# Kernel tuning notes

Hardware: AMD Instinct MI355X
Metric: run time of the kernel (lower is better)

Reference implementation:

```python
import jax, jax.numpy as jnp
import numpy as np

DIM = 1024
NUM_HEADS = 16
HEAD_DIM = DIM // NUM_HEADS


def setup_inputs() -> dict:
    key = jax.random.key(0)
    k1, k2, k3 = jax.random.split(key, 3)
    x = jax.random.normal(k1, (2, 2048, DIM), dtype=jnp.float32)
    # nn.Linear weights stored as [out, in]; apply as x @ W.T
    w_qkv = jax.random.normal(k2, (3 * DIM, DIM), dtype=jnp.float32) * (1.0 / np.sqrt(DIM))
    w_out = jax.random.normal(k3, (DIM, DIM), dtype=jnp.float32) * (1.0 / np.sqrt(DIM))
    return {"x": x, "w_qkv": w_qkv, "w_out": w_out}


def reference(x, w_qkv, w_out):
    b, t, _ = x.shape
    qkv = x @ w_qkv.T                                  # [b, t, 3*dim]
    qkv = qkv.reshape(b, t, 3, NUM_HEADS, HEAD_DIM)    # (three h d) split order
    q, k, v = jnp.moveaxis(qkv, 2, 0)                  # each [b, t, h, d]
    q = q.transpose(0, 2, 1, 3)                        # [b, h, t, d]
    k = k.transpose(0, 2, 1, 3)
    v = v.transpose(0, 2, 1, 3)
    attn = jnp.einsum('bhid,bhjd->bhij', q, k) / np.sqrt(HEAD_DIM)
    causal_mask = jnp.triu(jnp.ones((t, t), dtype=bool), k=1)
    attn = jnp.where(causal_mask, -jnp.inf, attn)
    attn = jax.nn.softmax(attn, axis=-1)
    out = jnp.einsum('bhij,bhjd->bhid', attn, v)
    out = out.transpose(0, 2, 1, 3).reshape(b, t, DIM)
    return out @ w_out.T
```

## Files before the change

### kernel.cpp

```cpp
#include <hip/hip_runtime.h>

#define DIM_ 1024
#define HEADS_ 16
#define HD_ 64
#define T_ 2048
#define BATCH_ 2
#define QKVN_ 3072

typedef unsigned short u16;
typedef unsigned int u32;
typedef float f32x4 __attribute__((ext_vector_type(4)));
typedef float f32x16 __attribute__((ext_vector_type(16)));
typedef short s16x8 __attribute__((ext_vector_type(8)));
typedef unsigned short u16x4 __attribute__((ext_vector_type(4)));

__device__ __forceinline__ u16 f2bf(float f) {
  unsigned u = __float_as_uint(f);
  u += 0x7fffu + ((u >> 16) & 1u);
  return (u16)(u >> 16);
}

__device__ __forceinline__ float fexp2(float x) {
  float r;
  asm("v_exp_f32 %0, %1" : "=v"(r) : "v"(x));
  return r;
}

__device__ __forceinline__ float fmax3(float a, float b, float c) {
  float r;
  asm("v_max3_f32 %0, %1, %2, %3" : "=v"(r) : "v"(a), "v"(b), "v"(c));
  return r;
}

__device__ __forceinline__ u32 cvtpk(float a, float b) {
  u32 r;
  asm("v_cvt_pk_bf16_f32 %0, %1, %2" : "=v"(r) : "v"(a), "v"(b));
  return r;
}

__global__ __launch_bounds__(256) void cvt_all(const float* __restrict__ x,
                                               const float* __restrict__ wqkv,
                                               const float* __restrict__ wout,
                                               u16* __restrict__ outbase) {
  int i = blockIdx.x * 256 + threadIdx.x;
  const float4* src;
  int off;
  if (i < 1048576) { src = (const float4*)x; off = i; }
  else if (i < 1835008) { src = (const float4*)wqkv; off = i - 1048576; }
  else { src = (const float4*)wout; off = i - 1835008; }
  float4 v = src[off];
  u16x4 o;
  o.x = f2bf(v.x); o.y = f2bf(v.y); o.z = f2bf(v.z); o.w = f2bf(v.w);
  reinterpret_cast<u16x4*>(outbase)[i] = o;
}

__device__ __forceinline__ void gld_lds16(const void* g, void* l) {
  auto gp = (__attribute__((address_space(1))) char*)(unsigned long long)g;
  auto lp = (__attribute__((address_space(3))) char*)(unsigned int)(unsigned long long)l;
  __builtin_amdgcn_global_load_lds(gp, lp, 16, 0, 0);
}

template <int MODE>
__global__ __launch_bounds__(256) void gemm1(const u16* __restrict__ A,
                                             const u16* __restrict__ B,
                                             void* __restrict__ Cv,
                                             u16* __restrict__ vto) {
  constexpr int K = 1024;
  constexpr int NN = (MODE == 1) ? 1024 : QKVN_;
  constexpr int NT = (MODE == 1) ? 8 : 24;
  constexpr int CPX = (MODE == 1) ? 32 : 96;
  __shared__ __align__(16) u16 smem[16384];
  u16* As = smem;
  u16* Bs = smem + 8192;
  const int bid = blockIdx.x;
  const int wk = (bid & 7) * CPX + (bid >> 3);
  const int mt = wk / NT, nt = wk % NT;
  const int tid = threadIdx.x;
  const int lane = tid & 63;
  const int w = tid >> 6;
  const int wr = w >> 1, wc = w & 1;
  const int lrow = lane & 15, kg = lane >> 4;
  const u16* Ag = A + (size_t)(mt * 128) * K;
  const u16* Bg = B + (size_t)(nt * 128) * K;

  f32x4 acc[4][4];
#pragma unroll
  for (int i = 0; i < 4; ++i)
#pragma unroll
    for (int j = 0; j < 4; ++j) {
      f32x4 z = {0.f, 0.f, 0.f, 0.f};
      acc[i][j] = z;
    }

  const int srow = tid >> 3;
  const int scol = 8 * ((tid & 7) ^ ((tid >> 3) & 7));
  const int ldsw = (tid & ~63) * 16;

  int aoff[4][2], boff[4][2];
#pragma unroll
  for (int mf = 0; mf < 4; ++mf)
#pragma unroll
    for (int ks = 0; ks < 2; ++ks) {
      aoff[mf][ks] = (wr * 64 + mf * 16 + lrow) * 128 + (((ks * 4 + kg) ^ (lrow & 7)) << 4);
      boff[mf][ks] = (wc * 64 + mf * 16 + lrow) * 128 + (((ks * 4 + kg) ^ (lrow & 7)) << 4);
    }

  for (int k0 = 0; k0 < K; k0 += 64) {
#pragma unroll
    for (int c = 0; c < 4; ++c) {
      gld_lds16(Ag + (size_t)(c * 32 + srow) * K + k0 + scol, (char*)As + c * 4096 + ldsw);
      gld_lds16(Bg + (size_t)(c * 32 + srow) * K + k0 + scol, (char*)Bs + c * 4096 + ldsw);
    }
    __syncthreads();
#pragma unroll
    for (int ks = 0; ks < 2; ++ks) {
      s16x8 a[4], b[4];
#pragma unroll
      for (int mf = 0; mf < 4; ++mf)
        a[mf] = *(const s16x8*)((const char*)As + aoff[mf][ks]);
#pragma unroll
      for (int nf = 0; nf < 4; ++nf)
        b[nf] = *(const s16x8*)((const char*)Bs + boff[nf][ks]);
#pragma unroll
      for (int mf = 0; mf < 4; ++mf)
#pragma unroll
        for (int nf = 0; nf < 4; ++nf)
          acc[mf][nf] = __builtin_amdgcn_mfma_f32_16x16x32_bf16(a[mf], b[nf], acc[mf][nf], 0, 0, 0);
    }
    __syncthreads();
  }

  if (MODE == 1) {
    float* C = (float*)Cv;
#pragma unroll
    for (int mf = 0; mf < 4; ++mf)
#pragma unroll
      for (int nf = 0; nf < 4; ++nf)
#pragma unroll
        for (int j = 0; j < 4; ++j) {
          int r = mt * 128 + wr * 64 + mf * 16 + 4 * kg + j;
          int c = nt * 128 + wc * 64 + nf * 16 + lrow;
          C[(size_t)r * NN + c] = acc[mf][nf][j];
        }
  } else if (nt < 16) {
    u16* qkvo = (u16*)Cv;
#pragma unroll
    for (int mf = 0; mf < 4; ++mf)
#pragma unroll
      for (int nf = 0; nf < 4; ++nf)
#pragma unroll
        for (int j = 0; j < 4; ++j) {
          int r = mt * 128 + wr * 64 + mf * 16 + 4 * kg + j;
          int c = nt * 128 + wc * 64 + nf * 16 + lrow;
          qkvo[(size_t)r * QKVN_ + c] = f2bf(acc[mf][nf][j]);
        }
  } else {
    const int c16 = tid >> 4, chunk = tid & 15;
    const int bb = mt >> 4;
    const int tb = (mt & 15) * 128 + chunk * 8;
#pragma unroll
    for (int p = 0; p < 2; ++p) {
      __syncthreads();
      if (wc == p) {
#pragma unroll
        for (int mf = 0; mf < 4; ++mf)
#pragma unroll
          for (int nf = 0; nf < 4; ++nf) {
            const int cl = nf * 16 + lrow;
            const int rl = wr * 64 + mf * 16 + 4 * kg;
            u16x4 pk;
            pk.x = f2bf(acc[mf][nf][0]); pk.y = f2bf(acc[mf][nf][1]);
            pk.z = f2bf(acc[mf][nf][2]); pk.w = f2bf(acc[mf][nf][3]);
            *(u16x4*)&smem[cl * 136 + rl] = pk;
          }
      }
      __syncthreads();
#pragma unroll
      for (int pp = 0; pp < 4; ++pp) {
        const int cl = pp * 16 + c16;
        const int cg = nt * 128 + p * 64 + cl;
        const int hV = (cg >> 6) & 15, d = cg & 63;
        const s16x8 v = *(const s16x8*)&smem[cl * 136 + chunk * 8];
        *(s16x8*)(vto + ((size_t)((bb * 16 + hV) * 64 + d)) * T_ + tb) = v;
      }
    }
  }
}

__global__ __launch_bounds__(256) void attn_fwd(const u16* __restrict__ qkv,
                                                const u16* __restrict__ vt,
                                                u16* __restrict__ o) {
  const int gid = blockIdx.x;
  const int jt = 31 - (gid >> 5);
  const int bh = gid & 31;
  const int b = bh >> 4, h = bh & 15;
  const int tid = threadIdx.x;
  const int lane = tid & 63;
  const int qw = (tid >> 6) & 1;
  const int kvg = tid >> 7;
  const int l31 = lane & 31, hi = lane >> 5;
  const int nt = jt + 1;
  const int nrt = (nt + 1) >> 1;
  const int qrow0 = 64 * jt + 32 * qw;

  __shared__ __align__(16) char smem[32768];

  const int row0s = tid >> 3, col0s = 8 * ((tid & 7) ^ ((tid >> 3) & 7));
  const int row1s = (256 + tid) >> 3, col1s = 8 * ((tid & 7) ^ (((256 + tid) >> 3) & 7));
  const u16* Kbase = qkv + (size_t)(b * T_) * QKVN_ + 1024 + h * 64;
  const u16* Ks0 = Kbase + (size_t)row0s * QKVN_ + col0s;
  const u16* Ks1 = Kbase + (size_t)row1s * QKVN_ + col1s;
  const int wbase = (tid & ~63) * 16;

  const u16* Vg = vt + (size_t)(bh * 64 + l31) * T_ + 8 * hi;

  const int rbyte = l31 * 128;
  const int xsw = l31 & 7;
  const float CEXP = 0.18033688011112042f;

  s16x8 qf[4];
  {
    const u16* qp = qkv + (size_t)(b * T_ + qrow0 + l31) * QKVN_ + h * 64 + 8 * hi;
#pragma unroll
    for (int ksl = 0; ksl < 4; ++ksl)
      qf[ksl] = *(const s16x8*)(qp + 16 * ksl);
  }

  f32x16 o0v, o1v;
#pragma unroll
  for (int r = 0; r < 16; ++r) { o0v[r] = 0.f; o1v[r] = 0.f; }
  float mrun = -__builtin_inff(), lrun = 0.0f;

  gld_lds16(Ks0, smem + wbase);
  gld_lds16(Ks1, smem + 4096 + wbase);
  if (nt > 1) {
    gld_lds16(Ks0 + (size_t)64 * QKVN_, smem + 16384 + wbase);
    gld_lds16(Ks1 + (size_t)64 * QKVN_, smem + 16384 + 4096 + wbase);
  }
  __syncthreads();

  int cur = 0;
  for (int r = 0; r < nrt; ++r) {
    const int t = 2 * r + kvg;
    if (2 * r + 2 < nt) {
      const size_t ko = (size_t)(2 * r + 2) * 64 * QKVN_;
      gld_lds16(Ks0 + ko, smem + (cur ^ 1) * 8192 + wbase);
      gld_lds16(Ks1 + ko, smem + (cur ^ 1) * 8192 + 4096 + wbase);
    }
    if (2 * r + 3 < nt) {
      const size_t ko = (size_t)(2 * r + 3) * 64 * QKVN_;
      gld_lds16(Ks0 + ko, smem + 16384 + (cur ^ 1) * 8192 + wbase);
      gld_lds16(Ks1 + ko, smem + 16384 + (cur ^ 1) * 8192 + 4096 + wbase);
    }

    if (t < nt) {
      const char* Kc = smem + kvg * 16384 + cur * 8192;
      const bool isdiag = (t == nt - 1);
      const bool two = !(isdiag && qw == 0);

      s16x8 vf0[4], vf1[4];
      const u16* Vt = Vg + t * 64;
#pragma unroll
      for (int kk = 0; kk < 4; ++kk) {
        vf0[kk] = *(const s16x8*)(Vt + 16 * kk);
        vf1[kk] = *(const s16x8*)(Vt + (size_t)32 * T_ + 16 * kk);
      }

      f32x16 s0v, s1v;
#pragma unroll
      for (int rr = 0; rr < 16; ++rr) { s0v[rr] = 0.f; s1v[rr] = 0.f; }
      __builtin_amdgcn_s_setprio(1);
#pragma unroll
      for (int ksl = 0; ksl < 4; ++ksl) {
        const s16x8 kf = *(const s16x8*)(Kc + rbyte + (((2 * ksl + hi) ^ xsw) << 4));
        s0v = __builtin_amdgcn_mfma_f32_32x32x16_bf16(kf, qf[ksl], s0v, 0, 0, 0);
      }
      if (two) {
#pragma unroll
        for (int ksl = 0; ksl < 4; ++ksl) {
          const s16x8 kf = *(const s16x8*)(Kc + 4096 + rbyte + (((2 * ksl + hi) ^ xsw) << 4));
          s1v = __builtin_amdgcn_mfma_f32_32x32x16_bf16(kf, qf[ksl], s1v, 0, 0, 0);
        }
      }
      __builtin_amdgcn_s_setprio(0);

      if (isdiag) {
        const int thr = 32 * qw + l31;
#pragma unroll
        for (int rr = 0; rr < 16; ++rr) {
          const int kvl = 4 * hi + (rr & 3) + 8 * (rr >> 2);
          if (kvl > thr) s0v[rr] = -__builtin_inff();
          if (two && kvl + 32 > thr) s1v[rr] = -__builtin_inff();
        }
      }

      float mloc = fmax3(s0v[0], s0v[1], s0v[2]);
#pragma unroll
      for (int rr = 3; rr < 15; rr += 2) mloc = fmax3(mloc, s0v[rr], s0v[rr + 1]);
      mloc = fmaxf(mloc, s0v[15]);
      if (two) {
        mloc = fmax3(mloc, s1v[0], s1v[1]);
#pragma unroll
        for (int rr = 2; rr < 16; rr += 2) mloc = fmax3(mloc, s1v[rr], s1v[rr + 1]);
      }
      mloc = fmaxf(mloc, __shfl_xor(mloc, 32));

      const bool needfull = !((mloc - mrun) * CEXP <= 8.0f);
      if (__any(needfull)) {
        const float newm = fmaxf(mrun, mloc);
        const float sc = fexp2((mrun - newm) * CEXP);
        mrun = newm;
        lrun *= sc;
        o0v *= sc;
        o1v *= sc;
      }
      const float msc = mrun * CEXP;

      float rs = 0.0f;
      u32 pd0[8], pd1[8];
#pragma unroll
      for (int ri = 0; ri < 8; ++ri) {
        const float p0 = fexp2(__builtin_fmaf(s0v[2 * ri], CEXP, -msc));
        const float p1 = fexp2(__builtin_fmaf(s0v[2 * ri + 1], CEXP, -msc));
        rs += p0 + p1;
        pd0[ri] = cvtpk(p0, p1);
      }
      if (two) {
#pragma unroll
        for (int ri = 0; ri < 8; ++ri) {
          const float p0 = fexp2(__builtin_fmaf(s1v[2 * ri], CEXP, -msc));
          const float p1 = fexp2(__builtin_fmaf(s1v[2 * ri + 1], CEXP, -msc));
          rs += p0 + p1;
          pd1[ri] = cvtpk(p0, p1);
        }
      }
      rs += __shfl_xor(rs, 32);
      lrun += rs;

      __builtin_amdgcn_s_setprio(1);
#pragma unroll
      for (int kk = 0; kk < 4; ++kk) {
        if (kk >= 2 && !two) break;
        u32 x0, y0, x1, y1;
        if (kk == 0)      { x0 = pd0[0]; y0 = pd0[2]; x1 = pd0[1]; y1 = pd0[3]; }
        else if (kk == 1) { x0 = pd0[4]; y0 = pd0[6]; x1 = pd0[5]; y1 = pd0[7]; }
        else if (kk == 2) { x0 = pd1[0]; y0 = pd1[2]; x1 = pd1[1]; y1 = pd1[3]; }
        else              { x0 = pd1[4]; y0 = pd1[6]; x1 = pd1[5]; y1 = pd1[7]; }
        asm volatile("v_permlane32_swap_b32 %0, %1" : "+v"(x0), "+v"(y0));
        asm volatile("v_permlane32_swap_b32 %0, %1" : "+v"(x1), "+v"(y1));
        u32 pw[4] = {x0, x1, y0, y1};
        const s16x8 pf = *(const s16x8*)pw;
        o0v = __builtin_amdgcn_mfma_f32_32x32x16_bf16(vf0[kk], pf, o0v, 0, 0, 0);
        o1v = __builtin_amdgcn_mfma_f32_32x32x16_bf16(vf1[kk], pf, o1v, 0, 0, 0);
      }
      __builtin_amdgcn_s_setprio(0);
    }

    __syncthreads();
    cur ^= 1;
  }

  float* Om = (float*)smem + qw * 2048;
  float* Mf = (float*)(smem + 16384) + qw * 64;
  float* Lf = (float*)(smem + 16896) + qw * 64;
  if (kvg == 1) {
#pragma unroll
    for (int rr = 0; rr < 16; ++rr) {
      Om[rr * 64 + lane] = o0v[rr];
      Om[(16 + rr) * 64 + lane] = o1v[rr];
    }
    Mf[lane] = mrun;
    Lf[lane] = lrun;
  }
  __syncthreads();
  if (kvg == 0) {
    const float mA = Mf[lane];
    const float lA = Lf[lane];
    const float m2 = fmaxf(mrun, mA);
    const float sB = fexp2((mrun - m2) * CEXP);
    const float sA = fexp2((mA - m2) * CEXP);
    const float linv = 1.0f / (lrun * sB + lA * sA);
    u16* orow = o + (size_t)(b * T_ + qrow0 + l31) * DIM_ + h * 64;
#pragma unroll
    for (int ri = 0; ri < 8; ++ri) {
      const int dbase0 = 4 * hi + 8 * (ri >> 1) + 2 * (ri & 1);
      const float a0 = (o0v[2 * ri] * sB + Om[(2 * ri) * 64 + lane] * sA) * linv;
      const float a1 = (o0v[2 * ri + 1] * sB + Om[(2 * ri + 1) * 64 + lane] * sA) * linv;
      const float c0 = (o1v[2 * ri] * sB + Om[(16 + 2 * ri) * 64 + lane] * sA) * linv;
      const float c1 = (o1v[2 * ri + 1] * sB + Om[(16 + 2 * ri + 1) * 64 + lane] * sA) * linv;
      *(u32*)(orow + dbase0) = cvtpk(a0, a1);
      *(u32*)(orow + 32 + dbase0) = cvtpk(c0, c1);
    }
  }
}

extern "C" void kernel_launch(void* const* d_in, const int* in_sizes, int n_in,
                              void* d_out, int out_size, void* d_ws, size_t ws_size,
                              hipStream_t stream) {
  const float* x = (const float*)d_in[0];
  const float* w_qkv = (const float*)d_in[1];
  const float* w_out = (const float*)d_in[2];
  char* ws = (char*)d_ws;
  u16* xb    = (u16*)(ws + 0);
  u16* wqkvb = (u16*)(ws + 8388608);
  u16* woutb = (u16*)(ws + 14680064);
  u16* qkvb  = (u16*)(ws + 16777216);
  u16* vtb   = (u16*)(ws + 41943040);
  u16* attno = (u16*)(ws + 50331648);

  cvt_all<<<8192, 256, 0, stream>>>(x, w_qkv, w_out, xb);
  gemm1<2><<<768, 256, 0, stream>>>(xb, wqkvb, qkvb, vtb);
  attn_fwd<<<1024, 256, 0, stream>>>(qkvb, vtb, attno);
  gemm1<1><<<256, 256, 0, stream>>>(attno, woutb, d_out, nullptr);
}
```

Baseline: 107.8 us.

## Pair causal query tiles per block and stage V through LDS

Each attention block now handles two query tiles, a long one and a short one (jt = 31-pr and pr), so every block does a near-equal amount of causal work. The grid halves to 512 blocks. V tiles are now loaded into a double-buffered LDS region with the async global-to-LDS path, the same way K is, instead of being read per-thread from global memory. LDS use grows to 64KB and launch bounds request 2 blocks per CU, which may cap registers and limit occupancy, and the fixed 512-block grid may underfill the GPU's compute units.

```diff
diff --git a/kernel.cpp b/kernel.cpp
--- a/kernel.cpp
+++ b/kernel.cpp
@@ -187,11 +187,11 @@
   }
 }
 
-__global__ __launch_bounds__(256) void attn_fwd(const u16* __restrict__ qkv,
-                                                const u16* __restrict__ vt,
-                                                u16* __restrict__ o) {
+__global__ __launch_bounds__(256, 2) void attn_fwd(const u16* __restrict__ qkv,
+                                                   const u16* __restrict__ vt,
+                                                   u16* __restrict__ o) {
   const int gid = blockIdx.x;
-  const int jt = 31 - (gid >> 5);
+  const int pr = gid >> 5;
   const int bh = gid & 31;
   const int b = bh >> 4, h = bh & 15;
   const int tid = threadIdx.x;
@@ -199,197 +199,212 @@
   const int qw = (tid >> 6) & 1;
   const int kvg = tid >> 7;
   const int l31 = lane & 31, hi = lane >> 5;
-  const int nt = jt + 1;
-  const int nrt = (nt + 1) >> 1;
-  const int qrow0 = 64 * jt + 32 * qw;
-
-  __shared__ __align__(16) char smem[32768];
-
-  const int row0s = tid >> 3, col0s = 8 * ((tid & 7) ^ ((tid >> 3) & 7));
-  const int row1s = (256 + tid) >> 3, col1s = 8 * ((tid & 7) ^ (((256 + tid) >> 3) & 7));
+
+  __shared__ __align__(16) char smem[65536];
+
+  const int row0s = tid >> 3;
+  const int cols = 8 * ((tid & 7) ^ (row0s & 7));
   const u16* Kbase = qkv + (size_t)(b * T_) * QKVN_ + 1024 + h * 64;
-  const u16* Ks0 = Kbase + (size_t)row0s * QKVN_ + col0s;
-  const u16* Ks1 = Kbase + (size_t)row1s * QKVN_ + col1s;
+  const u16* Vbase = vt + (size_t)(bh * 64) * T_;
+  const u16* Ks0 = Kbase + (size_t)row0s * QKVN_ + cols;
+  const u16* Ks1 = Kbase + (size_t)(32 + row0s) * QKVN_ + cols;
+  const u16* Vs0 = Vbase + (size_t)row0s * T_ + cols;
+  const u16* Vs1 = Vbase + (size_t)(32 + row0s) * T_ + cols;
   const int wbase = (tid & ~63) * 16;
-
-  const u16* Vg = vt + (size_t)(bh * 64 + l31) * T_ + 8 * hi;
 
   const int rbyte = l31 * 128;
   const int xsw = l31 & 7;
   const float CEXP = 0.18033688011112042f;
 
-  s16x8 qf[4];
-  {
-    const u16* qp = qkv + (size_t)(b * T_ + qrow0 + l31) * QKVN_ + h * 64 + 8 * hi;
-#pragma unroll
-    for (int ksl = 0; ksl < 4; ++ksl)
-      qf[ksl] = *(const s16x8*)(qp + 16 * ksl);
-  }
-
-  f32x16 o0v, o1v;
-#pragma unroll
-  for (int r = 0; r < 16; ++r) { o0v[r] = 0.f; o1v[r] = 0.f; }
-  float mrun = -__builtin_inff(), lrun = 0.0f;
-
-  gld_lds16(Ks0, smem + wbase);
-  gld_lds16(Ks1, smem + 4096 + wbase);
-  if (nt > 1) {
-    gld_lds16(Ks0 + (size_t)64 * QKVN_, smem + 16384 + wbase);
-    gld_lds16(Ks1 + (size_t)64 * QKVN_, smem + 16384 + 4096 + wbase);
-  }
-  __syncthreads();
-
-  int cur = 0;
-  for (int r = 0; r < nrt; ++r) {
-    const int t = 2 * r + kvg;
-    if (2 * r + 2 < nt) {
-      const size_t ko = (size_t)(2 * r + 2) * 64 * QKVN_;
-      gld_lds16(Ks0 + ko, smem + (cur ^ 1) * 8192 + wbase);
-      gld_lds16(Ks1 + ko, smem + (cur ^ 1) * 8192 + 4096 + wbase);
-    }
-    if (2 * r + 3 < nt) {
-      const size_t ko = (size_t)(2 * r + 3) * 64 * QKVN_;
-      gld_lds16(Ks0 + ko, smem + 16384 + (cur ^ 1) * 8192 + wbase);
-      gld_lds16(Ks1 + ko, smem + 16384 + (cur ^ 1) * 8192 + 4096 + wbase);
-    }
-
-    if (t < nt) {
-      const char* Kc = smem + kvg * 16384 + cur * 8192;
-      const bool isdiag = (t == nt - 1);
-      const bool two = !(isdiag && qw == 0);
-
-      s16x8 vf0[4], vf1[4];
-      const u16* Vt = Vg + t * 64;
-#pragma unroll
-      for (int kk = 0; kk < 4; ++kk) {
-        vf0[kk] = *(const s16x8*)(Vt + 16 * kk);
-        vf1[kk] = *(const s16x8*)(Vt + (size_t)32 * T_ + 16 * kk);
-      }
-
-      f32x16 s0v, s1v;
-#pragma unroll
-      for (int rr = 0; rr < 16; ++rr) { s0v[rr] = 0.f; s1v[rr] = 0.f; }
-      __builtin_amdgcn_s_setprio(1);
-#pragma unroll
-      for (int ksl = 0; ksl < 4; ++ksl) {
-        const s16x8 kf = *(const s16x8*)(Kc + rbyte + (((2 * ksl + hi) ^ xsw) << 4));
-        s0v = __builtin_amdgcn_mfma_f32_32x32x16_bf16(kf, qf[ksl], s0v, 0, 0, 0);
-      }
-      if (two) {
+  for (int ph = 0; ph < 2; ++ph) {
+    const int jt = (ph == 0) ? (31 - pr) : pr;
+    const int nt = jt + 1;
+    const int nrt = (nt + 1) >> 1;
+    const int qrow0 = 64 * jt + 32 * qw;
+
+    s16x8 qf[4];
+    {
+      const u16* qp = qkv + (size_t)(b * T_ + qrow0 + l31) * QKVN_ + h * 64 + 8 * hi;
+#pragma unroll
+      for (int ksl = 0; ksl < 4; ++ksl)
+        qf[ksl] = *(const s16x8*)(qp + 16 * ksl);
+    }
+
+    f32x16 o0v, o1v;
+#pragma unroll
+    for (int r = 0; r < 16; ++r) { o0v[r] = 0.f; o1v[r] = 0.f; }
+    float mrun = -__builtin_inff(), lrun = 0.0f;
+
+    __syncthreads();
+    gld_lds16(Ks0, smem + wbase);
+    gld_lds16(Ks1, smem + 4096 + wbase);
+    gld_lds16(Vs0, smem + 32768 + wbase);
+    gld_lds16(Vs1, smem + 32768 + 4096 + wbase);
+    if (nt > 1) {
+      const size_t ko = (size_t)64 * QKVN_;
+      gld_lds16(Ks0 + ko, smem + 8192 + wbase);
+      gld_lds16(Ks1 + ko, smem + 8192 + 4096 + wbase);
+      gld_lds16(Vs0 + 64, smem + 32768 + 8192 + wbase);
+      gld_lds16(Vs1 + 64, smem + 32768 + 8192 + 4096 + wbase);
+    }
+
+    int cur = 0;
+    for (int r = 0; r < nrt; ++r) {
+      const int t = 2 * r + kvg;
+      __syncthreads();
+
+      if (2 * r + 2 < nt) {
+        const size_t ko = (size_t)(2 * r + 2) * 64 * QKVN_;
+        const int vo = (2 * r + 2) * 64;
+        const int nb = (cur ^ 1) * 16384;
+        gld_lds16(Ks0 + ko, smem + nb + wbase);
+        gld_lds16(Ks1 + ko, smem + nb + 4096 + wbase);
+        gld_lds16(Vs0 + vo, smem + 32768 + nb + wbase);
+        gld_lds16(Vs1 + vo, smem + 32768 + nb + 4096 + wbase);
+      }
+      if (2 * r + 3 < nt) {
+        const size_t ko = (size_t)(2 * r + 3) * 64 * QKVN_;
+        const int vo = (2 * r + 3) * 64;
+        const int nb = (cur ^ 1) * 16384 + 8192;
+        gld_lds16(Ks0 + ko, smem + nb + wbase);
+        gld_lds16(Ks1 + ko, smem + nb + 4096 + wbase);
+        gld_lds16(Vs0 + vo, smem + 32768 + nb + wbase);
+        gld_lds16(Vs1 + vo, smem + 32768 + nb + 4096 + wbase);
+      }
+
+      if (t < nt) {
+        const char* Kc = smem + cur * 16384 + kvg * 8192;
+        const char* Vc = smem + 32768 + cur * 16384 + kvg * 8192;
+        const bool isdiag = (t == nt - 1);
+        const bool two = !(isdiag && qw == 0);
+
+        f32x16 s0v, s1v;
+#pragma unroll
+        for (int rr = 0; rr < 16; ++rr) { s0v[rr] = 0.f; s1v[rr] = 0.f; }
+        __builtin_amdgcn_s_setprio(1);
 #pragma unroll
         for (int ksl = 0; ksl < 4; ++ksl) {
-          const s16x8 kf = *(const s16x8*)(Kc + 4096 + rbyte + (((2 * ksl + hi) ^ xsw) << 4));
-          s1v = __builtin_amdgcn_mfma_f32_32x32x16_bf16(kf, qf[ksl], s1v, 0, 0, 0);
-        }
-      }
-      __builtin_amdgcn_s_setprio(0);
-
-      if (isdiag) {
-        const int thr = 32 * qw + l31;
-#pragma unroll
-        for (int rr = 0; rr < 16; ++rr) {
-          const int kvl = 4 * hi + (rr & 3) + 8 * (rr >> 2);
-          if (kvl > thr) s0v[rr] = -__builtin_inff();
-          if (two && kvl + 32 > thr) s1v[rr] = -__builtin_inff();
-        }
-      }
-
-      float mloc = fmax3(s0v[0], s0v[1], s0v[2]);
-#pragma unroll
-      for (int rr = 3; rr < 15; rr += 2) mloc = fmax3(mloc, s0v[rr], s0v[rr + 1]);
-      mloc = fmaxf(mloc, s0v[15]);
-      if (two) {
-        mloc = fmax3(mloc, s1v[0], s1v[1]);
-#pragma unroll
-        for (int rr = 2; rr < 16; rr += 2) mloc = fmax3(mloc, s1v[rr], s1v[rr + 1]);
-      }
-      mloc = fmaxf(mloc, __shfl_xor(mloc, 32));
-
-      const bool needfull = !((mloc - mrun) * CEXP <= 8.0f);
-      if (__any(needfull)) {
-        const float newm = fmaxf(mrun, mloc);
-        const float sc = fexp2((mrun - newm) * CEXP);
-        mrun = newm;
-        lrun *= sc;
-        o0v *= sc;
-        o1v *= sc;
-      }
-      const float msc = mrun * CEXP;
-
-      float rs = 0.0f;
-      u32 pd0[8], pd1[8];
+          const s16x8 kf = *(const s16x8*)(Kc + rbyte + (((2 * ksl + hi) ^ xsw) << 4));
+          s0v = __builtin_amdgcn_mfma_f32_32x32x16_bf16(kf, qf[ksl], s0v, 0, 0, 0);
+        }
+        if (two) {
+#pragma unroll
+          for (int ksl = 0; ksl < 4; ++ksl) {
+            const s16x8 kf = *(const s16x8*)(Kc + 4096 + rbyte + (((2 * ksl + hi) ^ xsw) << 4));
+            s1v = __builtin_amdgcn_mfma_f32_32x32x16_bf16(kf, qf[ksl], s1v, 0, 0, 0);
+          }
+        }
+        __builtin_amdgcn_s_setprio(0);
+
+        if (isdiag) {
+          const int thr = 32 * qw + l31;
+#pragma unroll
+          for (int rr = 0; rr < 16; ++rr) {
+            const int kvl = 4 * hi + (rr & 3) + 8 * (rr >> 2);
+            if (kvl > thr) s0v[rr] = -__builtin_inff();
+            if (two && kvl + 32 > thr) s1v[rr] = -__builtin_inff();
+          }
+        }
+
+        float mloc = fmax3(s0v[0], s0v[1], s0v[2]);
+#pragma unroll
+        for (int rr = 3; rr < 15; rr += 2) mloc = fmax3(mloc, s0v[rr], s0v[rr + 1]);
+        mloc = fmaxf(mloc, s0v[15]);
+        if (two) {
+          mloc = fmax3(mloc, s1v[0], s1v[1]);
+#pragma unroll
+          for (int rr = 2; rr < 16; rr += 2) mloc = fmax3(mloc, s1v[rr], s1v[rr + 1]);
+        }
+        mloc = fmaxf(mloc, __shfl_xor(mloc, 32));
+
+        const bool needfull = !((mloc - mrun) * CEXP <= 8.0f);
+        if (__any(needfull)) {
+          const float newm = fmaxf(mrun, mloc);
+          const float sc = fexp2((mrun - newm) * CEXP);
+          mrun = newm;
+          lrun *= sc;
+          o0v *= sc;
+          o1v *= sc;
+        }
+        const float msc = mrun * CEXP;
+
+        float rs = 0.0f;
+        u32 pd0[8], pd1[8];
+#pragma unroll
+        for (int ri = 0; ri < 8; ++ri) {
+          const float p0 = fexp2(__builtin_fmaf(s0v[2 * ri], CEXP, -msc));
+          const float p1 = fexp2(__builtin_fmaf(s0v[2 * ri + 1], CEXP, -msc));
+          rs += p0 + p1;
+          pd0[ri] = cvtpk(p0, p1);
+        }
+        if (two) {
+#pragma unroll
+          for (int ri = 0; ri < 8; ++ri) {
+            const float p0 = fexp2(__builtin_fmaf(s1v[2 * ri], CEXP, -msc));
+            const float p1 = fexp2(__builtin_fmaf(s1v[2 * ri + 1], CEXP, -msc));
+            rs += p0 + p1;
+            pd1[ri] = cvtpk(p0, p1);
+          }
+        }
+        rs += __shfl_xor(rs, 32);
+        lrun += rs;
+
+        __builtin_amdgcn_s_setprio(1);
+#pragma unroll
+        for (int kk = 0; kk < 4; ++kk) {
+          if (kk >= 2 && !two) break;
+          u32 x0, y0, x1, y1;
+          if (kk == 0)      { x0 = pd0[0]; y0 = pd0[2]; x1 = pd0[1]; y1 = pd0[3]; }
+          else if (kk == 1) { x0 = pd0[4]; y0 = pd0[6]; x1 = pd0[5]; y1 = pd0[7]; }
+          else if (kk == 2) { x0 = pd1[0]; y0 = pd1[2]; x1 = pd1[1]; y1 = pd1[3]; }
+          else              { x0 = pd1[4]; y0 = pd1[6]; x1 = pd1[5]; y1 = pd1[7]; }
+          asm volatile("v_permlane32_swap_b32 %0, %1" : "+v"(x0), "+v"(y0));
+          asm volatile("v_permlane32_swap_b32 %0, %1" : "+v"(x1), "+v"(y1));
+          u32 pw[4] = {x0, x1, y0, y1};
+          const s16x8 pf = *(const s16x8*)pw;
+          const s16x8 vf0 = *(const s16x8*)(Vc + rbyte + (((2 * kk + hi) ^ xsw) << 4));
+          const s16x8 vf1 = *(const s16x8*)(Vc + 4096 + rbyte + (((2 * kk + hi) ^ xsw) << 4));
+          o0v = __builtin_amdgcn_mfma_f32_32x32x16_bf16(vf0, pf, o0v, 0, 0, 0);
+          o1v = __builtin_amdgcn_mfma_f32_32x32x16_bf16(vf1, pf, o1v, 0, 0, 0);
+        }
+        __builtin_amdgcn_s_setprio(0);
+      }
+
+      cur ^= 1;
+    }
+
+    __syncthreads();
+    float* Om = (float*)smem + qw * 2048;
+    float* Mf = (float*)(smem + 16384) + qw * 64;
+    float* Lf = (float*)(smem + 16896) + qw * 64;
+    if (kvg == 1) {
+#pragma unroll
+      for (int rr = 0; rr < 16; ++rr) {
+        Om[rr * 64 + lane] = o0v[rr];
+        Om[(16 + rr) * 64 + lane] = o1v[rr];
+      }
+      Mf[lane] = mrun;
+      Lf[lane] = lrun;
+    }
+    __syncthreads();
+    if (kvg == 0) {
+      const float mA = Mf[lane];
+      const float lA = Lf[lane];
+      const float m2 = fmaxf(mrun, mA);
+      const float sB = fexp2((mrun - m2) * CEXP);
+      const float sA = fexp2((mA - m2) * CEXP);
+      const float linv = 1.0f / (lrun * sB + lA * sA);
+      u16* orow = o + (size_t)(b * T_ + qrow0 + l31) * DIM_ + h * 64;
 #pragma unroll
       for (int ri = 0; ri < 8; ++ri) {
-        const float p0 = fexp2(__builtin_fmaf(s0v[2 * ri], CEXP, -msc));
-        const float p1 = fexp2(__builtin_fmaf(s0v[2 * ri + 1], CEXP, -msc));
-        rs += p0 + p1;
-        pd0[ri] = cvtpk(p0, p1);
-      }
-      if (two) {
-#pragma unroll
-        for (int ri = 0; ri < 8; ++ri) {
-          const float p0 = fexp2(__builtin_fmaf(s1v[2 * ri], CEXP, -msc));
-          const float p1 = fexp2(__builtin_fmaf(s1v[2 * ri + 1], CEXP, -msc));
-          rs += p0 + p1;
-          pd1[ri] = cvtpk(p0, p1);
-        }
-      }
-      rs += __shfl_xor(rs, 32);
-      lrun += rs;
-
-      __builtin_amdgcn_s_setprio(1);
-#pragma unroll
-      for (int kk = 0; kk < 4; ++kk) {
-        if (kk >= 2 && !two) break;
-        u32 x0, y0, x1, y1;
-        if (kk == 0)      { x0 = pd0[0]; y0 = pd0[2]; x1 = pd0[1]; y1 = pd0[3]; }
-        else if (kk == 1) { x0 = pd0[4]; y0 = pd0[6]; x1 = pd0[5]; y1 = pd0[7]; }
-        else if (kk == 2) { x0 = pd1[0]; y0 = pd1[2]; x1 = pd1[1]; y1 = pd1[3]; }
-        else              { x0 = pd1[4]; y0 = pd1[6]; x1 = pd1[5]; y1 = pd1[7]; }
-        asm volatile("v_permlane32_swap_b32 %0, %1" : "+v"(x0), "+v"(y0));
-        asm volatile("v_permlane32_swap_b32 %0, %1" : "+v"(x1), "+v"(y1));
-        u32 pw[4] = {x0, x1, y0, y1};
-        const s16x8 pf = *(const s16x8*)pw;
-        o0v = __builtin_amdgcn_mfma_f32_32x32x16_bf16(vf0[kk], pf, o0v, 0, 0, 0);
-        o1v = __builtin_amdgcn_mfma_f32_32x32x16_bf16(vf1[kk], pf, o1v, 0, 0, 0);
-      }
-      __builtin_amdgcn_s_setprio(0);
-    }
-
-    __syncthreads();
-    cur ^= 1;
-  }
-
-  float* Om = (float*)smem + qw * 2048;
-  float* Mf = (float*)(smem + 16384) + qw * 64;
-  float* Lf = (float*)(smem + 16896) + qw * 64;
-  if (kvg == 1) {
-#pragma unroll
-    for (int rr = 0; rr < 16; ++rr) {
-      Om[rr * 64 + lane] = o0v[rr];
-      Om[(16 + rr) * 64 + lane] = o1v[rr];
-    }
-    Mf[lane] = mrun;
-    Lf[lane] = lrun;
-  }
-  __syncthreads();
-  if (kvg == 0) {
-    const float mA = Mf[lane];
-    const float lA = Lf[lane];
-    const float m2 = fmaxf(mrun, mA);
-    const float sB = fexp2((mrun - m2) * CEXP);
-    const float sA = fexp2((mA - m2) * CEXP);
-    const float linv = 1.0f / (lrun * sB + lA * sA);
-    u16* orow = o + (size_t)(b * T_ + qrow0 + l31) * DIM_ + h * 64;
-#pragma unroll
-    for (int ri = 0; ri < 8; ++ri) {
-      const int dbase0 = 4 * hi + 8 * (ri >> 1) + 2 * (ri & 1);
-      const float a0 = (o0v[2 * ri] * sB + Om[(2 * ri) * 64 + lane] * sA) * linv;
-      const float a1 = (o0v[2 * ri + 1] * sB + Om[(2 * ri + 1) * 64 + lane] * sA) * linv;
-      const float c0 = (o1v[2 * ri] * sB + Om[(16 + 2 * ri) * 64 + lane] * sA) * linv;
-      const float c1 = (o1v[2 * ri + 1] * sB + Om[(16 + 2 * ri + 1) * 64 + lane] * sA) * linv;
-      *(u32*)(orow + dbase0) = cvtpk(a0, a1);
-      *(u32*)(orow + 32 + dbase0) = cvtpk(c0, c1);
+        const int dbase0 = 4 * hi + 8 * (ri >> 1) + 2 * (ri & 1);
+        const float a0 = (o0v[2 * ri] * sB + Om[(2 * ri) * 64 + lane] * sA) * linv;
+        const float a1 = (o0v[2 * ri + 1] * sB + Om[(2 * ri + 1) * 64 + lane] * sA) * linv;
+        const float c0 = (o1v[2 * ri] * sB + Om[(16 + 2 * ri) * 64 + lane] * sA) * linv;
+        const float c1 = (o1v[2 * ri + 1] * sB + Om[(16 + 2 * ri + 1) * 64 + lane] * sA) * linv;
+        *(u32*)(orow + dbase0) = cvtpk(a0, a1);
+        *(u32*)(orow + 32 + dbase0) = cvtpk(c0, c1);
+      }
     }
   }
 }
@@ -410,6 +425,6 @@
 
   cvt_all<<<8192, 256, 0, stream>>>(x, w_qkv, w_out, xb);
   gemm1<2><<<768, 256, 0, stream>>>(xb, wqkvb, qkvb, vtb);
-  attn_fwd<<<1024, 256, 0, stream>>>(qkvb, vtb, attno);
+  attn_fwd<<<512, 256, 0, stream>>>(qkvb, vtb, attno);
   gemm1<1><<<256, 256, 0, stream>>>(attno, woutb, d_out, nullptr);
 }
```

After: 99.61 us. 7.6% less time.

## Pair causal query tiles per block and split KV across four wave groups

Applied to the files above, without the earlier changes.

The attention kernel now runs 512 threads per block. Each block handles two query tiles (jt and 31-jt) in sequence, which balances causal work across blocks and halves the grid to 512 blocks. KV tiles are split four ways across wave groups instead of two, with a 64KB double-buffered K staging area and a four-way softmax merge through shared memory at the end. This trades more LDS use and reduction overhead, plus possibly fewer resident blocks per CU, for better load balance and more KV parallelism per query tile.

```diff
diff --git a/kernel.cpp b/kernel.cpp
--- a/kernel.cpp
+++ b/kernel.cpp
@@ -187,29 +187,26 @@
   }
 }
 
-__global__ __launch_bounds__(256) void attn_fwd(const u16* __restrict__ qkv,
-                                                const u16* __restrict__ vt,
-                                                u16* __restrict__ o) {
+__global__ __launch_bounds__(512, 2) void attn_fwd(const u16* __restrict__ qkv,
+                                                   const u16* __restrict__ vt,
+                                                   u16* __restrict__ o) {
   const int gid = blockIdx.x;
-  const int jt = 31 - (gid >> 5);
+  const int pr = gid >> 5;
   const int bh = gid & 31;
   const int b = bh >> 4, h = bh & 15;
   const int tid = threadIdx.x;
   const int lane = tid & 63;
-  const int qw = (tid >> 6) & 1;
-  const int kvg = tid >> 7;
+  const int w = tid >> 6;
+  const int qw = w >> 2;
+  const int kvg = w & 3;
   const int l31 = lane & 31, hi = lane >> 5;
-  const int nt = jt + 1;
-  const int nrt = (nt + 1) >> 1;
-  const int qrow0 = 64 * jt + 32 * qw;
-
-  __shared__ __align__(16) char smem[32768];
-
-  const int row0s = tid >> 3, col0s = 8 * ((tid & 7) ^ ((tid >> 3) & 7));
-  const int row1s = (256 + tid) >> 3, col1s = 8 * ((tid & 7) ^ (((256 + tid) >> 3) & 7));
+
+  __shared__ __align__(16) char smem[65536];
+
+  const int rows = tid >> 3;
+  const int cols = 8 * ((tid & 7) ^ (rows & 7));
   const u16* Kbase = qkv + (size_t)(b * T_) * QKVN_ + 1024 + h * 64;
-  const u16* Ks0 = Kbase + (size_t)row0s * QKVN_ + col0s;
-  const u16* Ks1 = Kbase + (size_t)row1s * QKVN_ + col1s;
+  const u16* Ksrc = Kbase + (size_t)rows * QKVN_ + cols;
   const int wbase = (tid & ~63) * 16;
 
   const u16* Vg = vt + (size_t)(bh * 64 + l31) * T_ + 8 * hi;
@@ -218,178 +215,198 @@
   const int xsw = l31 & 7;
   const float CEXP = 0.18033688011112042f;
 
-  s16x8 qf[4];
-  {
-    const u16* qp = qkv + (size_t)(b * T_ + qrow0 + l31) * QKVN_ + h * 64 + 8 * hi;
-#pragma unroll
-    for (int ksl = 0; ksl < 4; ++ksl)
-      qf[ksl] = *(const s16x8*)(qp + 16 * ksl);
-  }
-
-  f32x16 o0v, o1v;
-#pragma unroll
-  for (int r = 0; r < 16; ++r) { o0v[r] = 0.f; o1v[r] = 0.f; }
-  float mrun = -__builtin_inff(), lrun = 0.0f;
-
-  gld_lds16(Ks0, smem + wbase);
-  gld_lds16(Ks1, smem + 4096 + wbase);
-  if (nt > 1) {
-    gld_lds16(Ks0 + (size_t)64 * QKVN_, smem + 16384 + wbase);
-    gld_lds16(Ks1 + (size_t)64 * QKVN_, smem + 16384 + 4096 + wbase);
-  }
-  __syncthreads();
-
-  int cur = 0;
-  for (int r = 0; r < nrt; ++r) {
-    const int t = 2 * r + kvg;
-    if (2 * r + 2 < nt) {
-      const size_t ko = (size_t)(2 * r + 2) * 64 * QKVN_;
-      gld_lds16(Ks0 + ko, smem + (cur ^ 1) * 8192 + wbase);
-      gld_lds16(Ks1 + ko, smem + (cur ^ 1) * 8192 + 4096 + wbase);
-    }
-    if (2 * r + 3 < nt) {
-      const size_t ko = (size_t)(2 * r + 3) * 64 * QKVN_;
-      gld_lds16(Ks0 + ko, smem + 16384 + (cur ^ 1) * 8192 + wbase);
-      gld_lds16(Ks1 + ko, smem + 16384 + (cur ^ 1) * 8192 + 4096 + wbase);
-    }
-
-    if (t < nt) {
-      const char* Kc = smem + kvg * 16384 + cur * 8192;
-      const bool isdiag = (t == nt - 1);
-      const bool two = !(isdiag && qw == 0);
-
-      s16x8 vf0[4], vf1[4];
-      const u16* Vt = Vg + t * 64;
-#pragma unroll
-      for (int kk = 0; kk < 4; ++kk) {
-        vf0[kk] = *(const s16x8*)(Vt + 16 * kk);
-        vf1[kk] = *(const s16x8*)(Vt + (size_t)32 * T_ + 16 * kk);
-      }
-
-      f32x16 s0v, s1v;
-#pragma unroll
-      for (int rr = 0; rr < 16; ++rr) { s0v[rr] = 0.f; s1v[rr] = 0.f; }
-      __builtin_amdgcn_s_setprio(1);
-#pragma unroll
-      for (int ksl = 0; ksl < 4; ++ksl) {
-        const s16x8 kf = *(const s16x8*)(Kc + rbyte + (((2 * ksl + hi) ^ xsw) << 4));
-        s0v = __builtin_amdgcn_mfma_f32_32x32x16_bf16(kf, qf[ksl], s0v, 0, 0, 0);
-      }
-      if (two) {
+  for (int ph = 0; ph < 2; ++ph) {
+    const int jt = (ph == 0) ? (31 - pr) : pr;
+    const int nt = jt + 1;
+    const int nrt = (nt + 3) >> 2;
+    const int qrow0 = 64 * jt + 32 * qw;
+
+    s16x8 qf[4];
+    {
+      const u16* qp = qkv + (size_t)(b * T_ + qrow0 + l31) * QKVN_ + h * 64 + 8 * hi;
+#pragma unroll
+      for (int ksl = 0; ksl < 4; ++ksl)
+        qf[ksl] = *(const s16x8*)(qp + 16 * ksl);
+    }
+
+    f32x16 o0v, o1v;
+#pragma unroll
+    for (int r = 0; r < 16; ++r) { o0v[r] = 0.f; o1v[r] = 0.f; }
+    float mrun = -__builtin_inff(), lrun = 0.0f;
+
+    __syncthreads();
+#pragma unroll
+    for (int par = 0; par < 4; ++par)
+      if (par < nt)
+        gld_lds16(Ksrc + (size_t)(par * 64) * QKVN_, smem + par * 8192 + wbase);
+
+    int cur = 0;
+    for (int r = 0; r < nrt; ++r) {
+      const int t = 4 * r + kvg;
+      __syncthreads();
+
+#pragma unroll
+      for (int par = 0; par < 4; ++par) {
+        const int tn = 4 * r + 4 + par;
+        if (tn < nt)
+          gld_lds16(Ksrc + (size_t)(tn * 64) * QKVN_,
+                    smem + (cur ^ 1) * 32768 + par * 8192 + wbase);
+      }
+
+      if (t < nt) {
+        const char* Kc = smem + cur * 32768 + kvg * 8192;
+        const bool isdiag = (t == nt - 1);
+        const bool two = !(isdiag && qw == 0);
+
+        s16x8 vf0[4], vf1[4];
+        const u16* Vt = Vg + t * 64;
+#pragma unroll
+        for (int kk = 0; kk < 4; ++kk) {
+          vf0[kk] = *(const s16x8*)(Vt + 16 * kk);
+          vf1[kk] = *(const s16x8*)(Vt + (size_t)32 * T_ + 16 * kk);
+        }
+
+        f32x16 s0v, s1v;
+#pragma unroll
+        for (int rr = 0; rr < 16; ++rr) { s0v[rr] = 0.f; s1v[rr] = 0.f; }
+        __builtin_amdgcn_s_setprio(1);
 #pragma unroll
         for (int ksl = 0; ksl < 4; ++ksl) {
-          const s16x8 kf = *(const s16x8*)(Kc + 4096 + rbyte + (((2 * ksl + hi) ^ xsw) << 4));
-          s1v = __builtin_amdgcn_mfma_f32_32x32x16_bf16(kf, qf[ksl], s1v, 0, 0, 0);
-        }
-      }
-      __builtin_amdgcn_s_setprio(0);
-
-      if (isdiag) {
-        const int thr = 32 * qw + l31;
-#pragma unroll
-        for (int rr = 0; rr < 16; ++rr) {
-          const int kvl = 4 * hi + (rr & 3) + 8 * (rr >> 2);
-          if (kvl > thr) s0v[rr] = -__builtin_inff();
-          if (two && kvl + 32 > thr) s1v[rr] = -__builtin_inff();
-        }
-      }
-
-      float mloc = fmax3(s0v[0], s0v[1], s0v[2]);
-#pragma unroll
-      for (int rr = 3; rr < 15; rr += 2) mloc = fmax3(mloc, s0v[rr], s0v[rr + 1]);
-      mloc = fmaxf(mloc, s0v[15]);
-      if (two) {
-        mloc = fmax3(mloc, s1v[0], s1v[1]);
-#pragma unroll
-        for (int rr = 2; rr < 16; rr += 2) mloc = fmax3(mloc, s1v[rr], s1v[rr + 1]);
-      }
-      mloc = fmaxf(mloc, __shfl_xor(mloc, 32));
-
-      const bool needfull = !((mloc - mrun) * CEXP <= 8.0f);
-      if (__any(needfull)) {
-        const float newm = fmaxf(mrun, mloc);
-        const float sc = fexp2((mrun - newm) * CEXP);
-        mrun = newm;
-        lrun *= sc;
-        o0v *= sc;
-        o1v *= sc;
-      }
-      const float msc = mrun * CEXP;
-
-      float rs = 0.0f;
-      u32 pd0[8], pd1[8];
+          const s16x8 kf = *(const s16x8*)(Kc + rbyte + (((2 * ksl + hi) ^ xsw) << 4));
+          s0v = __builtin_amdgcn_mfma_f32_32x32x16_bf16(kf, qf[ksl], s0v, 0, 0, 0);
+        }
+        if (two) {
+#pragma unroll
+          for (int ksl = 0; ksl < 4; ++ksl) {
+            const s16x8 kf = *(const s16x8*)(Kc + 4096 + rbyte + (((2 * ksl + hi) ^ xsw) << 4));
+            s1v = __builtin_amdgcn_mfma_f32_32x32x16_bf16(kf, qf[ksl], s1v, 0, 0, 0);
+          }
+        }
+        __builtin_amdgcn_s_setprio(0);
+
+        if (isdiag) {
+          const int thr = 32 * qw + l31;
+#pragma unroll
+          for (int rr = 0; rr < 16; ++rr) {
+            const int kvl = 4 * hi + (rr & 3) + 8 * (rr >> 2);
+            if (kvl > thr) s0v[rr] = -__builtin_inff();
+            if (two && kvl + 32 > thr) s1v[rr] = -__builtin_inff();
+          }
+        }
+
+        float mloc = fmax3(s0v[0], s0v[1], s0v[2]);
+#pragma unroll
+        for (int rr = 3; rr < 15; rr += 2) mloc = fmax3(mloc, s0v[rr], s0v[rr + 1]);
+        mloc = fmaxf(mloc, s0v[15]);
+        if (two) {
+          mloc = fmax3(mloc, s1v[0], s1v[1]);
+#pragma unroll
+          for (int rr = 2; rr < 16; rr += 2) mloc = fmax3(mloc, s1v[rr], s1v[rr + 1]);
+        }
+        mloc = fmaxf(mloc, __shfl_xor(mloc, 32));
+
+        const bool needfull = !((mloc - mrun) * CEXP <= 8.0f);
+        if (__any(needfull)) {
+          const float newm = fmaxf(mrun, mloc);
+          const float sc = fexp2((mrun - newm) * CEXP);
+          mrun = newm;
+          lrun *= sc;
+          o0v *= sc;
+          o1v *= sc;
+        }
+        const float msc = mrun * CEXP;
+
+        float rs = 0.0f;
+        u32 pd0[8], pd1[8];
+#pragma unroll
+        for (int ri = 0; ri < 8; ++ri) {
+          const float p0 = fexp2(__builtin_fmaf(s0v[2 * ri], CEXP, -msc));
+          const float p1 = fexp2(__builtin_fmaf(s0v[2 * ri + 1], CEXP, -msc));
+          rs += p0 + p1;
+          pd0[ri] = cvtpk(p0, p1);
+        }
+        if (two) {
+#pragma unroll
+          for (int ri = 0; ri < 8; ++ri) {
+            const float p0 = fexp2(__builtin_fmaf(s1v[2 * ri], CEXP, -msc));
+            const float p1 = fexp2(__builtin_fmaf(s1v[2 * ri + 1], CEXP, -msc));
+            rs += p0 + p1;
+            pd1[ri] = cvtpk(p0, p1);
+          }
+        }
+        rs += __shfl_xor(rs, 32);
+        lrun += rs;
+
+        __builtin_amdgcn_s_setprio(1);
+#pragma unroll
+        for (int kk = 0; kk < 4; ++kk) {
+          if (kk >= 2 && !two) break;
+          u32 x0, y0, x1, y1;
+          if (kk == 0)      { x0 = pd0[0]; y0 = pd0[2]; x1 = pd0[1]; y1 = pd0[3]; }
+          else if (kk == 1) { x0 = pd0[4]; y0 = pd0[6]; x1 = pd0[5]; y1 = pd0[7]; }
+          else if (kk == 2) { x0 = pd1[0]; y0 = pd1[2]; x1 = pd1[1]; y1 = pd1[3]; }
+          else              { x0 = pd1[4]; y0 = pd1[6]; x1 = pd1[5]; y1 = pd1[7]; }
+          asm volatile("v_permlane32_swap_b32 %0, %1" : "+v"(x0), "+v"(y0));
+          asm volatile("v_permlane32_swap_b32 %0, %1" : "+v"(x1), "+v"(y1));
+          u32 pw[4] = {x0, x1, y0, y1};
+          const s16x8 pf = *(const s16x8*)pw;
+          o0v = __builtin_amdgcn_mfma_f32_32x32x16_bf16(vf0[kk], pf, o0v, 0, 0, 0);
+          o1v = __builtin_amdgcn_mfma_f32_32x32x16_bf16(vf1[kk], pf, o1v, 0, 0, 0);
+        }
+        __builtin_amdgcn_s_setprio(0);
+      }
+
+      cur ^= 1;
+    }
+
+    __syncthreads();
+    float* Mf = (float*)(smem + 49152);
+    float* Lf = (float*)(smem + 50688);
+    if (kvg != 0) {
+      float* Om = (float*)(smem + qw * 24576 + (kvg - 1) * 8192);
+#pragma unroll
+      for (int rr = 0; rr < 16; ++rr) {
+        Om[rr * 64 + lane] = o0v[rr];
+        Om[(16 + rr) * 64 + lane] = o1v[rr];
+      }
+      Mf[(qw * 3 + kvg - 1) * 64 + lane] = mrun;
+      Lf[(qw * 3 + kvg - 1) * 64 + lane] = lrun;
+    }
+    __syncthreads();
+    if (kvg == 0) {
+      float mp[3], lp[3];
+#pragma unroll
+      for (int p = 0; p < 3; ++p) {
+        mp[p] = Mf[(qw * 3 + p) * 64 + lane];
+        lp[p] = Lf[(qw * 3 + p) * 64 + lane];
+      }
+      float m2 = mrun;
+#pragma unroll
+      for (int p = 0; p < 3; ++p) m2 = fmaxf(m2, mp[p]);
+      const float s0 = fexp2((mrun - m2) * CEXP);
+      float ltot = lrun * s0;
+      float sp[3];
+#pragma unroll
+      for (int p = 0; p < 3; ++p) { sp[p] = fexp2((mp[p] - m2) * CEXP); ltot += lp[p] * sp[p]; }
+
+      float num[32];
+#pragma unroll
+      for (int rr = 0; rr < 16; ++rr) { num[rr] = o0v[rr] * s0; num[16 + rr] = o1v[rr] * s0; }
+#pragma unroll
+      for (int p = 0; p < 3; ++p) {
+        const float* Om = (const float*)(smem + qw * 24576 + p * 8192);
+#pragma unroll
+        for (int rr = 0; rr < 32; ++rr) num[rr] += Om[rr * 64 + lane] * sp[p];
+      }
+
+      const float linv = 1.0f / ltot;
+      u16* orow = o + (size_t)(b * T_ + qrow0 + l31) * DIM_ + h * 64;
 #pragma unroll
       for (int ri = 0; ri < 8; ++ri) {
-        const float p0 = fexp2(__builtin_fmaf(s0v[2 * ri], CEXP, -msc));
-        const float p1 = fexp2(__builtin_fmaf(s0v[2 * ri + 1], CEXP, -msc));
-        rs += p0 + p1;
-        pd0[ri] = cvtpk(p0, p1);
-      }
-      if (two) {
-#pragma unroll
-        for (int ri = 0; ri < 8; ++ri) {
-          const float p0 = fexp2(__builtin_fmaf(s1v[2 * ri], CEXP, -msc));
-          const float p1 = fexp2(__builtin_fmaf(s1v[2 * ri + 1], CEXP, -msc));
-          rs += p0 + p1;
-          pd1[ri] = cvtpk(p0, p1);
-        }
-      }
-      rs += __shfl_xor(rs, 32);
-      lrun += rs;
-
-      __builtin_amdgcn_s_setprio(1);
-#pragma unroll
-      for (int kk = 0; kk < 4; ++kk) {
-        if (kk >= 2 && !two) break;
-        u32 x0, y0, x1, y1;
-        if (kk == 0)      { x0 = pd0[0]; y0 = pd0[2]; x1 = pd0[1]; y1 = pd0[3]; }
-        else if (kk == 1) { x0 = pd0[4]; y0 = pd0[6]; x1 = pd0[5]; y1 = pd0[7]; }
-        else if (kk == 2) { x0 = pd1[0]; y0 = pd1[2]; x1 = pd1[1]; y1 = pd1[3]; }
-        else              { x0 = pd1[4]; y0 = pd1[6]; x1 = pd1[5]; y1 = pd1[7]; }
-        asm volatile("v_permlane32_swap_b32 %0, %1" : "+v"(x0), "+v"(y0));
-        asm volatile("v_permlane32_swap_b32 %0, %1" : "+v"(x1), "+v"(y1));
-        u32 pw[4] = {x0, x1, y0, y1};
-        const s16x8 pf = *(const s16x8*)pw;
-        o0v = __builtin_amdgcn_mfma_f32_32x32x16_bf16(vf0[kk], pf, o0v, 0, 0, 0);
-        o1v = __builtin_amdgcn_mfma_f32_32x32x16_bf16(vf1[kk], pf, o1v, 0, 0, 0);
-      }
-      __builtin_amdgcn_s_setprio(0);
-    }
-
-    __syncthreads();
-    cur ^= 1;
-  }
-
-  float* Om = (float*)smem + qw * 2048;
-  float* Mf = (float*)(smem + 16384) + qw * 64;
-  float* Lf = (float*)(smem + 16896) + qw * 64;
-  if (kvg == 1) {
-#pragma unroll
-    for (int rr = 0; rr < 16; ++rr) {
-      Om[rr * 64 + lane] = o0v[rr];
-      Om[(16 + rr) * 64 + lane] = o1v[rr];
-    }
-    Mf[lane] = mrun;
-    Lf[lane] = lrun;
-  }
-  __syncthreads();
-  if (kvg == 0) {
-    const float mA = Mf[lane];
-    const float lA = Lf[lane];
-    const float m2 = fmaxf(mrun, mA);
-    const float sB = fexp2((mrun - m2) * CEXP);
-    const float sA = fexp2((mA - m2) * CEXP);
-    const float linv = 1.0f / (lrun * sB + lA * sA);
-    u16* orow = o + (size_t)(b * T_ + qrow0 + l31) * DIM_ + h * 64;
-#pragma unroll
-    for (int ri = 0; ri < 8; ++ri) {
-      const int dbase0 = 4 * hi + 8 * (ri >> 1) + 2 * (ri & 1);
-      const float a0 = (o0v[2 * ri] * sB + Om[(2 * ri) * 64 + lane] * sA) * linv;
-      const float a1 = (o0v[2 * ri + 1] * sB + Om[(2 * ri + 1) * 64 + lane] * sA) * linv;
-      const float c0 = (o1v[2 * ri] * sB + Om[(16 + 2 * ri) * 64 + lane] * sA) * linv;
-      const float c1 = (o1v[2 * ri + 1] * sB + Om[(16 + 2 * ri + 1) * 64 + lane] * sA) * linv;
-      *(u32*)(orow + dbase0) = cvtpk(a0, a1);
-      *(u32*)(orow + 32 + dbase0) = cvtpk(c0, c1);
+        const int dbase0 = 4 * hi + 8 * (ri >> 1) + 2 * (ri & 1);
+        *(u32*)(orow + dbase0) = cvtpk(num[2 * ri] * linv, num[2 * ri + 1] * linv);
+        *(u32*)(orow + 32 + dbase0) = cvtpk(num[16 + 2 * ri] * linv, num[16 + 2 * ri + 1] * linv);
+      }
     }
   }
 }
@@ -410,6 +427,6 @@
 
   cvt_all<<<8192, 256, 0, stream>>>(x, w_qkv, w_out, xb);
   gemm1<2><<<768, 256, 0, stream>>>(xb, wqkvb, qkvb, vtb);
-  attn_fwd<<<1024, 256, 0, stream>>>(qkvb, vtb, attno);
+  attn_fwd<<<512, 512, 0, stream>>>(qkvb, vtb, attno);
   gemm1<1><<<256, 256, 0, stream>>>(attno, woutb, d_out, nullptr);
 }
```

New measurement: 118.1 us. 1.1x slower.
